# Kernel optimization log

Hardware: AMD Instinct MI355X
Metric: run time of the kernel (lower is better)

Reference implementation:

```python
import jax, jax.numpy as jnp
import numpy as np

D_MODEL = 768
D_STATE = 64
HEADDIM = 8
EXPAND = 2
D_CONV = 4
CHUNK = 128
D_INNER = EXPAND * D_MODEL            # 1536
NHEADS = D_INNER // HEADDIM           # 192
CONV_DIM = D_INNER + 2 * D_STATE      # 1664 (ngroups=1)
D_IN_PROJ = 2 * D_INNER + 2 * D_STATE + NHEADS  # 3392
BATCH = 2
SEQLEN = 1024


def setup_inputs() -> dict:
    key = jax.random.key(0)
    ks = jax.random.split(key, 8)
    x = jax.random.normal(ks[0], (BATCH, D_MODEL, SEQLEN), jnp.float32)
    W_in = jax.random.normal(ks[1], (D_IN_PROJ, D_MODEL), jnp.float32) / np.sqrt(D_MODEL)
    conv_w = jax.random.normal(ks[2], (CONV_DIM, D_CONV), jnp.float32) / np.sqrt(D_CONV)
    conv_b = jnp.zeros((CONV_DIM,), jnp.float32)
    # dt bias init: inverse softplus of dt ~ LogUniform[1e-3, 0.1] (mamba2 default)
    dt = jnp.exp(jax.random.uniform(ks[3], (NHEADS,)) * (np.log(0.1) - np.log(1e-3)) + np.log(1e-3))
    dt_bias = dt + jnp.log(-jnp.expm1(-dt))
    # A ~ Uniform[1.0, 1.1] per A_init_range, stored as log
    A_log = jnp.log(jax.random.uniform(ks[4], (NHEADS,), minval=1.0, maxval=1.1))
    D = jnp.ones((NHEADS,), jnp.float32)
    norm_w = jnp.ones((D_INNER,), jnp.float32)
    W_out = jax.random.normal(ks[5], (D_MODEL, D_INNER), jnp.float32) / np.sqrt(D_INNER)
    return dict(x=x, W_in=W_in, conv_w=conv_w, conv_b=conv_b, dt_bias=dt_bias,
                A_log=A_log, D=D, norm_w=norm_w, W_out=W_out)


def _segsum(t):
    # t: (..., T) -> (..., T, T) with [i,j] = sum_{k=j+1..i} t_k (i>=j), -inf above diag
    T = t.shape[-1]
    cs = jnp.cumsum(t, axis=-1)
    d = cs[..., :, None] - cs[..., None, :]
    mask = jnp.tril(jnp.ones((T, T), bool))
    return jnp.where(mask, d, -jnp.inf)


def _ssd(xh, dt, A, Bm, Cm):
    # xh: (b,l,h,p), dt: (b,l,h), A: (h,), Bm/Cm: (b,l,n) (ngroups=1)
    b, l, h, p = xh.shape
    c = l // CHUNK
    xh = xh.reshape(b, c, CHUNK, h, p)
    dt = dt.reshape(b, c, CHUNK, h)
    Bm = Bm.reshape(b, c, CHUNK, -1)
    Cm = Cm.reshape(b, c, CHUNK, -1)
    dA = jnp.transpose(dt * A, (0, 3, 1, 2))          # (b,h,c,Q)
    A_cs = jnp.cumsum(dA, axis=-1)                    # (b,h,c,Q)
    Lmat = jnp.exp(_segsum(dA))                       # (b,h,c,Q,Q) causal decay
    xdt = xh * dt[..., None]                          # (b,c,Q,h,p)
    # intra-chunk (diagonal blocks)
    scores = jnp.einsum('bcln,bcsn->bcls', Cm, Bm)
    Y_diag = jnp.einsum('bcls,bhcls,bcshp->bclhp', scores, Lmat, xdt)
    # chunk-final states
    decay_states = jnp.exp(A_cs[..., -1:] - A_cs)     # (b,h,c,Q)
    states = jnp.einsum('bcln,bhcl,bclhp->bchpn', Bm, decay_states, xdt)
    states = jnp.concatenate([jnp.zeros_like(states[:, :1]), states], axis=1)  # (b,c+1,h,p,n)
    # inter-chunk recurrence via decay matrix over chunks (c is small)
    dA_chunk = jnp.pad(A_cs[..., -1], ((0, 0), (0, 0), (1, 0)))  # (b,h,c+1)
    decay_chunk = jnp.exp(_segsum(dA_chunk))                     # (b,h,c+1,c+1)
    new_states = jnp.einsum('bhzc,bchpn->bzhpn', decay_chunk, states)
    prev = new_states[:, :-1]                         # (b,c,h,p,n) state entering each chunk
    Y_off = jnp.einsum('bcln,bchpn,bhcl->bclhp', Cm, prev, jnp.exp(A_cs))
    return (Y_diag + Y_off).reshape(b, l, h, p)


def _forward(x, W_in, conv_w, conv_b, dt_bias, A_log, D, norm_w, W_out):
    u = jnp.transpose(x, (0, 2, 1))                   # (b,l,d_model)
    zxbcdt = u @ W_in.T                               # (b,l,3392)
    z = zxbcdt[..., :D_INNER]
    xBC = zxbcdt[..., D_INNER:D_INNER + CONV_DIM]
    dt = jax.nn.softplus(zxbcdt[..., -NHEADS:] + dt_bias)
    # causal depthwise conv1d + silu
    xc = jnp.transpose(xBC, (0, 2, 1))                # (b,conv_dim,l)
    xc = jax.lax.conv_general_dilated(xc, conv_w[:, None, :], (1,),
                                      [(D_CONV - 1, 0)], feature_group_count=CONV_DIM)
    xBC = jax.nn.silu(jnp.transpose(xc, (0, 2, 1)) + conv_b)
    xs = xBC[..., :D_INNER]
    Bm = xBC[..., D_INNER:D_INNER + D_STATE]
    Cm = xBC[..., -D_STATE:]
    A = -jnp.exp(A_log)
    b, l, _ = xs.shape
    xh = xs.reshape(b, l, NHEADS, HEADDIM)
    y = _ssd(xh, dt, A, Bm, Cm) + D[None, None, :, None] * xh
    y = y.reshape(b, l, D_INNER)
    # RMSNormGated (norm_before_gate=False): gate then rmsnorm
    y = y * jax.nn.silu(z)
    y = y * jax.lax.rsqrt(jnp.mean(y * y, axis=-1, keepdims=True) + 1e-5) * norm_w
    out = y @ W_out.T
    return jnp.transpose(out, (0, 2, 1))              # back to (b, d_model, l)


def reference(x, W_in, conv_w, conv_b, dt_bias, A_log, D, norm_w, W_out):
    return _forward(x, W_in, conv_w, conv_b, dt_bias, A_log, D, norm_w, W_out)
```

## Files before the change

kernel.cpp:

```cpp
#include <hip/hip_runtime.h>
#include <cstddef>
#include <cstdint>


typedef __bf16 bf16_t;
typedef bf16_t bf16x2 __attribute__((ext_vector_type(2)));
typedef bf16_t bf16x4 __attribute__((ext_vector_type(4)));
typedef bf16_t bf16x8 __attribute__((ext_vector_type(8)));
typedef float f32x4 __attribute__((ext_vector_type(4)));

#define OFF_UB   ((size_t)0)
#define OFF_ZX   (OFF_UB  + 786432)
#define OFF_XBC  (OFF_ZX  + 3276800)
#define OFF_DT   (OFF_XBC + 1703936)
#define OFF_ACS  (OFF_DT  + 393216)
#define OFF_SC   (OFF_ACS + 393216)
#define OFF_ST   (OFF_SC  + 262144)
#define OFF_PV   (OFF_ST  + 1572864)
#define OFF_Y    (OFF_PV  + 786432)
#define OFF_Y2B  (OFF_Y   + 1572864)

__device__ __forceinline__ float siluf(float x) { return x / (1.f + __expf(-x)); }

__global__ __launch_bounds__(256) void transpose_x_kernel(const float* __restrict__ x,
                                                          bf16_t* __restrict__ ub) {
  __shared__ float tile[32][33];
  int b = blockIdx.z;
  int d0 = blockIdx.x * 32, l0 = blockIdx.y * 32;
  int tx = threadIdx.x & 31, ty = threadIdx.x >> 5;
  for (int r = ty; r < 32; r += 8)
    tile[r][tx] = x[((size_t)(b * 768 + d0 + r)) * 1024 + l0 + tx];
  __syncthreads();
  for (int r = ty; r < 32; r += 8)
    ub[((size_t)(b * 1024 + l0 + r)) * 768 + d0 + tx] = (bf16_t)tile[tx][r];
}

template <int MODE>
__global__ __launch_bounds__(256) void gemm_fused(const bf16_t* __restrict__ A,
                                                  const float* __restrict__ B32,
                                                  void* __restrict__ Cv,
                                                  float* __restrict__ dtb,
                                                  const float* __restrict__ dt_bias,
                                                  int K) {
  __shared__ __align__(16) float smemf[3072];
  bf16_t* Asmem = (bf16_t*)smemf;
  bf16_t* Bsmem = Asmem + 32 * 64;
  float* eps = smemf;

  int tid = threadIdx.x;
  int wave = tid >> 6, lane = tid & 63;
  int wr = wave >> 1, wc = wave & 1;

  int gx = gridDim.x, gy = gridDim.y;
  int nwg = gx * gy;
  int flat = blockIdx.y * gx + blockIdx.x;
  int q = nwg >> 3;
  int cm = (flat & 7) * q + (flat >> 3);
  int bx = cm / gy, by = cm % gy;
  int m0 = by * 32, n0 = bx * 64;

  const bf16_t* Ag = A + (size_t)m0 * K;

  int aofs; const bf16_t* agp;
  {
    int r = tid >> 3, c = tid & 7;
    aofs = r * 128 + ((c ^ (r & 7)) << 4);
    agp = Ag + (size_t)r * K + c * 8;
  }
  int bofs[2]; const float* bgp[2]; bool bval[2];
#pragma unroll
  for (int i = 0; i < 2; ++i) {
    int id = i * 256 + tid;
    int r = id >> 3, c = id & 7;
    bofs[i] = r * 128 + ((c ^ (r & 7)) << 4);
    int grow = n0 + r;
    bval[i] = (MODE == 1) || (grow < 3392);
    bgp[i] = B32 + (size_t)grow * K + c * 8;
  }

  f32x4 acc[2] = {};
  uint4 areg;
  float4 b0[2], b1[2];
  areg = *(const uint4*)(agp);
#pragma unroll
  for (int i = 0; i < 2; ++i) {
    if (bval[i]) {
      b0[i] = *(const float4*)(bgp[i]);
      b1[i] = *(const float4*)(bgp[i] + 4);
    } else {
      b0[i] = make_float4(0.f, 0.f, 0.f, 0.f);
      b1[i] = make_float4(0.f, 0.f, 0.f, 0.f);
    }
  }

  for (int k0 = 0; k0 < K; k0 += 64) {
    __syncthreads();
    *(uint4*)((char*)Asmem + aofs) = areg;
#pragma unroll
    for (int i = 0; i < 2; ++i) {
      bf16x8 o = {(bf16_t)b0[i].x, (bf16_t)b0[i].y, (bf16_t)b0[i].z, (bf16_t)b0[i].w,
                  (bf16_t)b1[i].x, (bf16_t)b1[i].y, (bf16_t)b1[i].z, (bf16_t)b1[i].w};
      *(bf16x8*)((char*)Bsmem + bofs[i]) = o;
    }
    __syncthreads();
    if (k0 + 64 < K) {
      areg = *(const uint4*)(agp + k0 + 64);
#pragma unroll
      for (int i = 0; i < 2; ++i) {
        if (bval[i]) {
          b0[i] = *(const float4*)(bgp[i] + k0 + 64);
          b1[i] = *(const float4*)(bgp[i] + k0 + 68);
        }
      }
    }
#pragma unroll
    for (int half = 0; half < 2; ++half) {
      int ca = half * 4 + (lane >> 4);
      bf16x8 af, bfr[2];
      {
        int Ra = wr * 16 + (lane & 15);
        af = *(const bf16x8*)((const char*)Asmem + Ra * 128 + ((ca ^ (Ra & 7)) << 4));
      }
#pragma unroll
      for (int f = 0; f < 2; ++f) {
        int Rb = wc * 32 + f * 16 + (lane & 15);
        bfr[f] = *(const bf16x8*)((const char*)Bsmem + Rb * 128 + ((ca ^ (Rb & 7)) << 4));
      }
#pragma unroll
      for (int j = 0; j < 2; ++j)
        acc[j] = __builtin_amdgcn_mfma_f32_16x16x32_bf16(af, bfr[j], acc[j], 0, 0, 0);
    }
  }

  __syncthreads();
  {
    int rl = wr * 16 + ((lane >> 4) << 2);
#pragma unroll
    for (int j = 0; j < 2; ++j) {
      int col = wc * 32 + j * 16 + (lane & 15);
#pragma unroll
      for (int rr = 0; rr < 4; ++rr)
        eps[(rl + rr) * 69 + col] = acc[j][rr];
    }
  }
  __syncthreads();
  if (MODE == 0) {
    if (n0 < 3200) {
      bf16_t* Cb = (bf16_t*)Cv;
#pragma unroll
      for (int r = 0; r < 2; ++r) {
        int idx = tid + r * 256;
        int row = idx >> 4, c4 = (idx & 15) << 2;
        float4 v = *(const float4*)&eps[row * 69 + c4];
        bf16x4 o = {(bf16_t)v.x, (bf16_t)v.y, (bf16_t)v.z, (bf16_t)v.w};
        *(bf16x4*)&Cb[(size_t)(m0 + row) * 3200 + n0 + c4] = o;
      }
    } else {
      int b = m0 >> 10, t0 = m0 & 1023;
#pragma unroll
      for (int cg = 0; cg < 2; ++cg) {
        int col = cg * 32 + (tid >> 3);
        int h = n0 + col - 3200;
        if (h < 192) {
          int rr = (tid & 7) * 4;
          float bias = dt_bias[h];
          float vv[4];
#pragma unroll
          for (int k = 0; k < 4; ++k) {
            float v = eps[(rr + k) * 69 + col] + bias;
            vv[k] = (v > 20.f) ? v : log1pf(__expf(v));
          }
          *(float4*)&dtb[((size_t)(b * 192 + h)) * 1024 + t0 + rr] =
              make_float4(vv[0], vv[1], vv[2], vv[3]);
        }
      }
    }
  } else {
    float* Cf = (float*)Cv;
    int b = m0 >> 10, l0 = m0 & 1023;
#pragma unroll
    for (int cg = 0; cg < 2; ++cg) {
      int col = cg * 32 + (tid >> 3);
      int rr = (tid & 7) * 4;
      float4 v = make_float4(eps[(rr + 0) * 69 + col], eps[(rr + 1) * 69 + col],
                             eps[(rr + 2) * 69 + col], eps[(rr + 3) * 69 + col]);
      *(float4*)&Cf[((size_t)(b * 768 + n0 + col)) * 1024 + l0 + rr] = v;
    }
  }
}

__global__ __launch_bounds__(128) void conv_kernel(const bf16_t* __restrict__ zxb,
                                                   const float* __restrict__ conv_w,
                                                   const float* __restrict__ conv_b,
                                                   bf16_t* __restrict__ xBC) {
  int ch2 = blockIdx.x * 128 + threadIdx.x;
  if (ch2 >= 832) return;
  int ch = ch2 * 2;
  int m = blockIdx.y;
  int b = m >> 10, l = m & 1023;
  float a0 = conv_b[ch], a1 = conv_b[ch + 1];
  const bf16_t* base = zxb + (size_t)b * 1024 * 3200 + 1536 + ch;
#pragma unroll
  for (int j = 0; j < 4; ++j) {
    int tj = l - 3 + j;
    if (tj >= 0) {
      bf16x2 v = *(const bf16x2*)&base[(size_t)tj * 3200];
      a0 = fmaf(conv_w[ch * 4 + j], (float)v[0], a0);
      a1 = fmaf(conv_w[(ch + 1) * 4 + j], (float)v[1], a1);
    }
  }
  bf16x2 o = {(bf16_t)siluf(a0), (bf16_t)siluf(a1)};
  *(bf16x2*)&xBC[(size_t)m * 1664 + ch] = o;
}

__global__ __launch_bounds__(128) void scan_kernel(const float* __restrict__ dtb,
                                                   const float* __restrict__ A_log,
                                                   float* __restrict__ Acs) {
  __shared__ float s[128];
  int idx = blockIdx.x;
  int c = idx & 7;
  int bh = idx >> 3;
  int h = bh % 192;
  int l = threadIdx.x;
  float Ah = -__expf(A_log[h]);
  float v = dtb[(size_t)bh * 1024 + c * 128 + l] * Ah;
  s[l] = v;
  __syncthreads();
  for (int off = 1; off < 128; off <<= 1) {
    float add = (l >= off) ? s[l - off] : 0.f;
    __syncthreads();
    s[l] += add;
    __syncthreads();
  }
  Acs[(size_t)idx * 128 + l] = s[l];
}

__global__ __launch_bounds__(256) void scores_kernel(const bf16_t* __restrict__ xBC,
                                                     float* __restrict__ scores) {
  __shared__ float Cs[16][16];
  __shared__ float Bs[16][128];
  int bc = blockIdx.x;
  int l0 = blockIdx.y * 16;
  const bf16_t* base = xBC + (size_t)bc * 128 * 1664;
  int tid = threadIdx.x;
  int tx = tid & 15, ty = tid >> 4;
  float acc[8] = {};
  for (int n0 = 0; n0 < 64; n0 += 16) {
    Cs[tid & 15][tid >> 4] =
        (float)base[(size_t)(l0 + (tid >> 4)) * 1664 + 1600 + n0 + (tid & 15)];
    for (int id = tid; id < 2048; id += 256) {
      int sr = id >> 4, nn = id & 15;
      Bs[nn][sr] = (float)base[(size_t)sr * 1664 + 1536 + n0 + nn];
    }
    __syncthreads();
#pragma unroll
    for (int nn = 0; nn < 16; ++nn) {
      float a = Cs[nn][ty];
#pragma unroll
      for (int j = 0; j < 8; ++j)
        acc[j] = fmaf(a, Bs[nn][tx * 8 + j], acc[j]);
    }
    __syncthreads();
  }
  float* srow = scores + (size_t)bc * 16384 + (size_t)(l0 + ty) * 128;
#pragma unroll
  for (int j = 0; j < 8; ++j) srow[tx * 8 + j] = acc[j];
}

__global__ __launch_bounds__(256) void states_mfma_kernel(
    const bf16_t* __restrict__ xBC, const float* __restrict__ dtb,
    const float* __restrict__ Acs, float* __restrict__ st2) {
  __shared__ bf16_t Asm[64 * 128];
  __shared__ bf16_t Wsm[128 * 128];
  __shared__ float dcoef[16][128];
  int tile = blockIdx.x;
  int bc = blockIdx.y;
  int c = bc & 7, b = bc >> 3;
  int hg0 = tile * 16;
  int tid = threadIdx.x;
  int wave = tid >> 6, lane = tid & 63;

#pragma unroll
  for (int i = 0; i < 8; ++i) {
    int id = tid + i * 256;
    int hh = id >> 7, s = id & 127;
    int h = hg0 + hh;
    const float* ar = Acs + (((size_t)(b * 192 + h)) * 8 + c) * 128;
    float dv = dtb[((size_t)(b * 192 + h)) * 1024 + c * 128 + s];
    dcoef[hh][s] = dv * __expf(ar[127] - ar[s]);
  }
#pragma unroll
  for (int i = 0; i < 32; ++i) {
    int id = tid + i * 256;
    int s = id >> 6, n = id & 63;
    float v = (float)xBC[((size_t)(bc * 128 + s)) * 1664 + 1536 + n];
    int byte = n * 256 + (((s >> 3) ^ (n & 7)) << 4) + (s & 7) * 2;
    *(bf16_t*)((char*)Asm + byte) = (bf16_t)v;
  }
  __syncthreads();
#pragma unroll
  for (int i = 0; i < 64; ++i) {
    int id = tid + i * 256;
    int s = id >> 7, hp = id & 127;
    float v = (float)xBC[((size_t)(bc * 128 + s)) * 1664 + hg0 * 8 + hp] * dcoef[hp >> 3][s];
    int byte = hp * 256 + (((s >> 3) ^ (hp & 7)) << 4) + (s & 7) * 2;
    *(bf16_t*)((char*)Wsm + byte) = (bf16_t)v;
  }
  __syncthreads();

  f32x4 acc[4][2] = {};
#pragma unroll
  for (int ks = 0; ks < 4; ++ks) {
    int cc = ks * 4 + (lane >> 4);
    bf16x8 af[4], bfr[2];
#pragma unroll
    for (int i = 0; i < 4; ++i) {
      int Ra = i * 16 + (lane & 15);
      af[i] = *(const bf16x8*)((const char*)Asm + Ra * 256 + ((cc ^ (Ra & 7)) << 4));
    }
#pragma unroll
    for (int j = 0; j < 2; ++j) {
      int Rb = wave * 32 + j * 16 + (lane & 15);
      bfr[j] = *(const bf16x8*)((const char*)Wsm + Rb * 256 + ((cc ^ (Rb & 7)) << 4));
    }
#pragma unroll
    for (int i = 0; i < 4; ++i)
#pragma unroll
      for (int j = 0; j < 2; ++j)
        acc[i][j] = __builtin_amdgcn_mfma_f32_16x16x32_bf16(af[i], bfr[j], acc[i][j], 0, 0, 0);
  }
#pragma unroll
  for (int i = 0; i < 4; ++i)
#pragma unroll
    for (int j = 0; j < 2; ++j) {
      int n = i * 16 + ((lane >> 4) << 2);
      int col = tile * 128 + wave * 32 + j * 16 + (lane & 15);
      float* sp = st2 + (size_t)bc * 98304 + (size_t)n * 1536 + col;
#pragma unroll
      for (int rr = 0; rr < 4; ++rr) sp[(size_t)rr * 1536] = acc[i][j][rr];
    }
}

__global__ __launch_bounds__(512) void recur_kernel(const float* __restrict__ Acs,
                                                    const float* __restrict__ states,
                                                    bf16_t* __restrict__ prev) {
  int bh = blockIdx.x;
  int b = bh / 192, h = bh % 192;
  int tid = threadIdx.x;
  int p = tid >> 6, n = tid & 63;
  float s_run = 0.f;
  for (int c = 0; c < 8; ++c) {
    size_t base = (size_t)(b * 8 + c) * 98304;
    prev[base + (size_t)(h * 8 + p) * 64 + n] = (bf16_t)s_run;
    float dAs = Acs[(((size_t)(b * 192 + h)) * 8 + c) * 128 + 127];
    s_run = s_run * __expf(dAs) + states[base + (size_t)n * 1536 + h * 8 + p];
  }
}

__global__ __launch_bounds__(128) void ydiag_off_kernel(
    const bf16_t* __restrict__ xBC, const float* __restrict__ dtb,
    const float* __restrict__ Acs, const float* __restrict__ scores,
    const bf16_t* __restrict__ pv, const float* __restrict__ Dvec,
    bf16_t* __restrict__ Y) {
  __shared__ float sc_s[128][36];
  __shared__ float xdtT[2][8][132];
  __shared__ float acs_s[2][128];
  __shared__ bf16_t pv_s[2][512];
  int idx = blockIdx.x;
  int hp2 = idx % 96;
  int bc = idx / 96;
  int h0 = hp2 * 2;
  int c = bc & 7, b = bc >> 3;
  int tid = threadIdx.x;
  int lane = tid & 63, wid = tid >> 6;

#pragma unroll
  for (int hh = 0; hh < 2; ++hh) {
    int h = h0 + hh;
    acs_s[hh][tid] = Acs[(((size_t)(b * 192 + h)) * 8 + c) * 128 + tid];
    {
      int p = tid & 7, s0 = (tid >> 3) * 8;
      const float* dtr = dtb + ((size_t)(b * 192 + h)) * 1024 + c * 128;
#pragma unroll
      for (int j = 0; j < 8; ++j) {
        int s = s0 + j;
        xdtT[hh][p][s] = (float)xBC[((size_t)(bc * 128 + s)) * 1664 + h * 8 + p] * dtr[s];
      }
    }
    {
      const bf16_t* pb = pv + (size_t)bc * 98304 + (size_t)h * 512;
      *(bf16x4*)&pv_s[hh][tid * 4] = *(const bf16x4*)&pb[tid * 4];
    }
  }

  f32x4 acc[2][4] = {};
  const float* sall = scores + (size_t)bc * 16384;
  for (int ks = 0; ks < 4; ++ks) {
    __syncthreads();
#pragma unroll
    for (int i = 0; i < 8; ++i) {
      int id = tid + i * 128;
      int l = id >> 3, c4 = (id & 7) * 4;
      *(float4*)&sc_s[l][c4] = *(const float4*)&sall[(size_t)l * 128 + ks * 32 + c4];
    }
    __syncthreads();

#pragma unroll
    for (int hh = 0; hh < 2; ++hh) {
      bf16x8 bfv;
      {
        int p = lane & 7;
        int sb = (lane >> 4) * 8;
        float4 v0 = *(const float4*)&xdtT[hh][p][ks * 32 + sb];
        float4 v1 = *(const float4*)&xdtT[hh][p][ks * 32 + sb + 4];
        bfv[0] = (bf16_t)v0.x; bfv[1] = (bf16_t)v0.y; bfv[2] = (bf16_t)v0.z; bfv[3] = (bf16_t)v0.w;
        bfv[4] = (bf16_t)v1.x; bfv[5] = (bf16_t)v1.y; bfv[6] = (bf16_t)v1.z; bfv[7] = (bf16_t)v1.w;
      }
#pragma unroll
      for (int mf = 0; mf < 4; ++mf) {
        int lbase = (mf * 2 + wid) * 16;
        if (ks * 32 > lbase + 15) continue;
        int l = lbase + (lane & 15);
        float al = acs_s[hh][l];
        int sb = (lane >> 4) * 8;
        int sg = ks * 32 + sb;
        float4 s0 = *(const float4*)&sc_s[l][sb];
        float4 s1 = *(const float4*)&sc_s[l][sb + 4];
        float4 e0 = *(const float4*)&acs_s[hh][sg];
        float4 e1 = *(const float4*)&acs_s[hh][sg + 4];
        float sv[8] = {s0.x, s0.y, s0.z, s0.w, s1.x, s1.y, s1.z, s1.w};
        float ev[8] = {e0.x, e0.y, e0.z, e0.w, e1.x, e1.y, e1.z, e1.w};
        bf16x8 af;
#pragma unroll
        for (int j = 0; j < 8; ++j) {
          float v = sv[j] * __expf(al - ev[j]);
          af[j] = (bf16_t)((sg + j <= l) ? v : 0.f);
        }
        acc[hh][mf] = __builtin_amdgcn_mfma_f32_16x16x32_bf16(af, bfv, acc[hh][mf], 0, 0, 0);
      }
    }
  }

  __syncthreads();
#pragma unroll
  for (int ks2 = 0; ks2 < 2; ++ks2) {
    int kbase = ks2 * 32 + (lane >> 4) * 8;
#pragma unroll
    for (int hh = 0; hh < 2; ++hh) {
      bf16x8 bv;
      {
        int p = lane & 15;
        if (p < 8) {
          bv = *(const bf16x8*)&pv_s[hh][p * 64 + kbase];
        } else {
          bv = (bf16x8)(bf16_t)0.f;
        }
      }
#pragma unroll
      for (int mf = 0; mf < 4; ++mf) {
        int l = (mf * 2 + wid) * 16 + (lane & 15);
        float el = __expf(acs_s[hh][l]);
        bf16x8 c8 = *(const bf16x8*)&xBC[((size_t)(bc * 128 + l)) * 1664 + 1600 + kbase];
        bf16x8 af;
#pragma unroll
        for (int j = 0; j < 8; ++j) af[j] = (bf16_t)((float)c8[j] * el);
        acc[hh][mf] = __builtin_amdgcn_mfma_f32_16x16x32_bf16(af, bv, acc[hh][mf], 0, 0, 0);
      }
    }
  }

  int p = lane & 15;
  if (p < 8) {
#pragma unroll
    for (int hh = 0; hh < 2; ++hh) {
      int h = h0 + hh;
      float Dh = Dvec[h];
      int rg = (lane >> 4) * 4;
#pragma unroll
      for (int mf = 0; mf < 4; ++mf) {
        int lbase = (mf * 2 + wid) * 16;
        bf16_t* yp = Y + ((size_t)(bc * 128 + lbase + rg)) * 1536 + h * 8 + p;
#pragma unroll
        for (int rr = 0; rr < 4; ++rr) {
          float xv = (float)xBC[((size_t)(bc * 128 + lbase + rg + rr)) * 1664 + h * 8 + p];
          yp[(size_t)rr * 1536] = (bf16_t)(acc[hh][mf][rr] + Dh * xv);
        }
      }
    }
  }
}

__global__ __launch_bounds__(256) void gatenorm_kernel(const bf16_t* __restrict__ Yb,
                                                       const bf16_t* __restrict__ zxb,
                                                       const float* __restrict__ norm_w,
                                                       bf16_t* __restrict__ y2b) {
  int m = blockIdx.x;
  int tid = threadIdx.x;
  int base = tid * 6;
  const bf16_t* yrow = Yb + (size_t)m * 1536 + base;
  const bf16_t* zrow = zxb + (size_t)m * 3200 + base;
  float vals[6];
  float ss = 0.f;
#pragma unroll
  for (int j = 0; j < 3; ++j) {
    bf16x2 yv = *(const bf16x2*)&yrow[j * 2];
    bf16x2 zv = *(const bf16x2*)&zrow[j * 2];
    float v0 = (float)yv[0] * siluf((float)zv[0]);
    float v1 = (float)yv[1] * siluf((float)zv[1]);
    vals[j * 2] = v0; vals[j * 2 + 1] = v1;
    ss = fmaf(v0, v0, fmaf(v1, v1, ss));
  }
#pragma unroll
  for (int off = 32; off > 0; off >>= 1) ss += __shfl_down(ss, off);
  __shared__ float red[4];
  int lane = tid & 63, wid = tid >> 6;
  if (lane == 0) red[wid] = ss;
  __syncthreads();
  float tot = red[0] + red[1] + red[2] + red[3];
  float scale = rsqrtf(tot * (1.f / 1536.f) + 1e-5f);
  bf16_t* orow = y2b + (size_t)m * 1536 + base;
#pragma unroll
  for (int j = 0; j < 3; ++j) {
    bf16x2 o = {(bf16_t)(vals[j * 2] * scale * norm_w[base + j * 2]),
                (bf16_t)(vals[j * 2 + 1] * scale * norm_w[base + j * 2 + 1])};
    *(bf16x2*)&orow[j * 2] = o;
  }
}

extern "C" void kernel_launch(void* const* d_in, const int* in_sizes, int n_in,
                              void* d_out, int out_size, void* d_ws, size_t ws_size,
                              hipStream_t stream) {
  const float* x = (const float*)d_in[0];
  const float* W_in = (const float*)d_in[1];
  const float* conv_w = (const float*)d_in[2];
  const float* conv_b = (const float*)d_in[3];
  const float* dt_bias = (const float*)d_in[4];
  const float* A_log = (const float*)d_in[5];
  const float* Dvec = (const float*)d_in[6];
  const float* norm_w = (const float*)d_in[7];
  const float* W_out = (const float*)d_in[8];
  float* out = (float*)d_out;
  float* ws = (float*)d_ws;

  bf16_t* ub = (bf16_t*)(ws + OFF_UB);
  bf16_t* zxb = (bf16_t*)(ws + OFF_ZX);
  bf16_t* xBC = (bf16_t*)(ws + OFF_XBC);
  float* dtb = ws + OFF_DT;
  float* Acs = ws + OFF_ACS;
  float* sc = ws + OFF_SC;
  float* st = ws + OFF_ST;
  bf16_t* pv = (bf16_t*)(ws + OFF_PV);
  bf16_t* Yb = (bf16_t*)(ws + OFF_Y);
  bf16_t* y2b = (bf16_t*)(ws + OFF_Y2B);

  transpose_x_kernel<<<dim3(24, 32, 2), 256, 0, stream>>>(x, ub);
  gemm_fused<0><<<dim3(54, 64), 256, 0, stream>>>(ub, W_in, zxb, dtb, dt_bias, 768);
  conv_kernel<<<dim3(7, 2048), 128, 0, stream>>>(zxb, conv_w, conv_b, xBC);
  scan_kernel<<<3072, 128, 0, stream>>>(dtb, A_log, Acs);
  scores_kernel<<<dim3(16, 8), 256, 0, stream>>>(xBC, sc);
  states_mfma_kernel<<<dim3(12, 16), 256, 0, stream>>>(xBC, dtb, Acs, st);
  recur_kernel<<<384, 512, 0, stream>>>(Acs, st, pv);
  ydiag_off_kernel<<<1536, 128, 0, stream>>>(xBC, dtb, Acs, sc, pv, Dvec, Yb);
  gatenorm_kernel<<<2048, 256, 0, stream>>>(Yb, zxb, norm_w, y2b);
  gemm_fused<1><<<dim3(12, 64), 256, 0, stream>>>(y2b, W_out, out, nullptr, nullptr, 1536);
}
```

Before: 151.6 us.

## Stream GEMM tiles directly into LDS with double buffering

Replaces the register-staged load/convert/store of A and B tiles with global_load_lds direct-to-LDS copies into a double-buffered shared memory area, keeping the B weights in fp32 in LDS and converting to bf16 at fragment-read time. This removes the register round trip and one barrier per k-step, and lets the next tile load overlap MFMA work. In exchange LDS use grows to 40KB, which may cut occupancy, and LDS traffic for B doubles because it is stored as fp32. Out-of-range B rows are clamped instead of zeroed.

```diff
diff --git a/kernel.cpp b/kernel.cpp
--- a/kernel.cpp
+++ b/kernel.cpp
@@ -8,6 +8,13 @@
 typedef bf16_t bf16x4 __attribute__((ext_vector_type(4)));
 typedef bf16_t bf16x8 __attribute__((ext_vector_type(8)));
 typedef float f32x4 __attribute__((ext_vector_type(4)));
+
+typedef const __attribute__((address_space(1))) unsigned int gu32;
+typedef __attribute__((address_space(3))) unsigned int lu32;
+
+__device__ __forceinline__ void gld16(const void* g, void* l) {
+  __builtin_amdgcn_global_load_lds((gu32*)g, (lu32*)l, 16, 0, 0);
+}
 
 #define OFF_UB   ((size_t)0)
 #define OFF_ZX   (OFF_UB  + 786432)
@@ -42,10 +49,8 @@
                                                   float* __restrict__ dtb,
                                                   const float* __restrict__ dt_bias,
                                                   int K) {
-  __shared__ __align__(16) float smemf[3072];
-  bf16_t* Asmem = (bf16_t*)smemf;
-  bf16_t* Bsmem = Asmem + 32 * 64;
-  float* eps = smemf;
+  __shared__ __align__(16) char smem[40960];
+  float* eps = (float*)smem;
 
   int tid = threadIdx.x;
   int wave = tid >> 6, lane = tid & 63;
@@ -61,75 +66,67 @@
 
   const bf16_t* Ag = A + (size_t)m0 * K;
 
-  int aofs; const bf16_t* agp;
+  const bf16_t* agp;
   {
-    int r = tid >> 3, c = tid & 7;
-    aofs = r * 128 + ((c ^ (r & 7)) << 4);
+    int r = tid >> 3, cs = tid & 7;
+    int c = cs ^ (r & 7);
     agp = Ag + (size_t)r * K + c * 8;
   }
-  int bofs[2]; const float* bgp[2]; bool bval[2];
-#pragma unroll
-  for (int i = 0; i < 2; ++i) {
-    int id = i * 256 + tid;
-    int r = id >> 3, c = id & 7;
-    bofs[i] = r * 128 + ((c ^ (r & 7)) << 4);
+  const float* bgp[4];
+#pragma unroll
+  for (int pp = 0; pp < 4; ++pp) {
+    int o = pp * 4096 + tid * 16;
+    int r = o >> 8, br = o & 255;
+    int cs = br >> 5, hf = (br >> 4) & 1;
+    int c = cs ^ (r & 7);
     int grow = n0 + r;
-    bval[i] = (MODE == 1) || (grow < 3392);
-    bgp[i] = B32 + (size_t)grow * K + c * 8;
+    if (MODE == 0 && grow > 3391) grow = 3391;
+    bgp[pp] = B32 + (size_t)grow * K + c * 8 + hf * 4;
   }
 
   f32x4 acc[2] = {};
-  uint4 areg;
-  float4 b0[2], b1[2];
-  areg = *(const uint4*)(agp);
-#pragma unroll
-  for (int i = 0; i < 2; ++i) {
-    if (bval[i]) {
-      b0[i] = *(const float4*)(bgp[i]);
-      b1[i] = *(const float4*)(bgp[i] + 4);
-    } else {
-      b0[i] = make_float4(0.f, 0.f, 0.f, 0.f);
-      b1[i] = make_float4(0.f, 0.f, 0.f, 0.f);
-    }
-  }
-
-  for (int k0 = 0; k0 < K; k0 += 64) {
-    __syncthreads();
-    *(uint4*)((char*)Asmem + aofs) = areg;
-#pragma unroll
-    for (int i = 0; i < 2; ++i) {
-      bf16x8 o = {(bf16_t)b0[i].x, (bf16_t)b0[i].y, (bf16_t)b0[i].z, (bf16_t)b0[i].w,
-                  (bf16_t)b1[i].x, (bf16_t)b1[i].y, (bf16_t)b1[i].z, (bf16_t)b1[i].w};
-      *(bf16x8*)((char*)Bsmem + bofs[i]) = o;
-    }
-    __syncthreads();
-    if (k0 + 64 < K) {
-      areg = *(const uint4*)(agp + k0 + 64);
-#pragma unroll
-      for (int i = 0; i < 2; ++i) {
-        if (bval[i]) {
-          b0[i] = *(const float4*)(bgp[i] + k0 + 64);
-          b1[i] = *(const float4*)(bgp[i] + k0 + 68);
-        }
-      }
-    }
+
+  int NS = K >> 6;
+  {
+    char* ab = smem;
+    gld16(agp, ab + tid * 16);
+#pragma unroll
+    for (int pp = 0; pp < 4; ++pp)
+      gld16(bgp[pp], ab + 4096 + pp * 4096 + tid * 16);
+  }
+  int cur = 0;
+  for (int s = 0; s < NS; ++s) {
+    __syncthreads();
+    if (s + 1 < NS) {
+      int k0n = (s + 1) * 64;
+      char* ab = smem + (cur ^ 1) * 20480;
+      gld16(agp + k0n, ab + tid * 16);
+#pragma unroll
+      for (int pp = 0; pp < 4; ++pp)
+        gld16(bgp[pp] + k0n, ab + 4096 + pp * 4096 + tid * 16);
+    }
+    const char* ab = smem + cur * 20480;
+    const char* bb = ab + 4096;
 #pragma unroll
     for (int half = 0; half < 2; ++half) {
       int ca = half * 4 + (lane >> 4);
-      bf16x8 af, bfr[2];
+      bf16x8 af;
       {
         int Ra = wr * 16 + (lane & 15);
-        af = *(const bf16x8*)((const char*)Asmem + Ra * 128 + ((ca ^ (Ra & 7)) << 4));
+        af = *(const bf16x8*)(ab + Ra * 128 + ((ca ^ (Ra & 7)) << 4));
       }
 #pragma unroll
       for (int f = 0; f < 2; ++f) {
         int Rb = wc * 32 + f * 16 + (lane & 15);
-        bfr[f] = *(const bf16x8*)((const char*)Bsmem + Rb * 128 + ((ca ^ (Rb & 7)) << 4));
-      }
-#pragma unroll
-      for (int j = 0; j < 2; ++j)
-        acc[j] = __builtin_amdgcn_mfma_f32_16x16x32_bf16(af, bfr[j], acc[j], 0, 0, 0);
-    }
+        const char* p = bb + Rb * 256 + ((ca ^ (Rb & 7)) << 5);
+        float4 x0 = *(const float4*)p;
+        float4 x1 = *(const float4*)(p + 16);
+        bf16x8 bf8 = {(bf16_t)x0.x, (bf16_t)x0.y, (bf16_t)x0.z, (bf16_t)x0.w,
+                      (bf16_t)x1.x, (bf16_t)x1.y, (bf16_t)x1.z, (bf16_t)x1.w};
+        acc[f] = __builtin_amdgcn_mfma_f32_16x16x32_bf16(af, bf8, acc[f], 0, 0, 0);
+      }
+    }
+    cur ^= 1;
   }
 
   __syncthreads();
```

After: 270.1 us. 78.2% more time.
